# Optimization experiments

Measured on AMD Instinct MI355X. Metric: run time of the kernel, lower is better.

The kernel has to match this reference:

```python
import jax, jax.numpy as jnp
import numpy as np

D = 1024

def setup_inputs() -> dict:
    key = jax.random.key(0)
    ks = jax.random.split(key, 7)
    s = 1.0 / np.sqrt(D)
    x = jax.random.normal(ks[0], (4, 4096, D), dtype=jnp.float32)
    Wi = jax.random.uniform(ks[1], (2 * D, D), jnp.float32, -s, s)   # in_proj weight [2D, D]
    bi = jax.random.uniform(ks[2], (2 * D,), jnp.float32, -s, s)
    Wc = jax.random.uniform(ks[3], (D, 1, 3), jnp.float32, -0.577, 0.577)  # depthwise conv [D,1,3]
    bc = jax.random.uniform(ks[4], (D,), jnp.float32, -0.577, 0.577)
    Wo = jax.random.uniform(ks[5], (D, D), jnp.float32, -s, s)       # out_proj weight [D, D]
    bo = jax.random.uniform(ks[6], (D,), jnp.float32, -s, s)
    return {"x": x, "Wi": Wi, "bi": bi, "Wc": Wc, "bc": bc, "Wo": Wo, "bo": bo}

def _depthwise_conv1d(v, Wc, bc):
    # v: [B, L, D] -> NCH [B, D, L]; kernel [D, 1, 3] (OIH), groups = D; pad 1 both sides
    y = jax.lax.conv_general_dilated(
        v.transpose(0, 2, 1), Wc,
        window_strides=(1,), padding=[(1, 1)],
        dimension_numbers=("NCH", "OIH", "NCH"),
        feature_group_count=v.shape[-1])
    return y.transpose(0, 2, 1) + bc  # [B, L, D]

def reference(x, Wi, bi, Wc, bc, Wo, bo):
    uv = jnp.einsum("bld,ed->ble", x, Wi) + bi        # [B, L, 2D]
    u, v = jnp.split(uv, 2, axis=-1)                   # each [B, L, D]
    y = _depthwise_conv1d(v, Wc, bc)
    y = jax.nn.silu(y) * u                             # fused gate
    return jnp.einsum("bld,ed->ble", y, Wo) + bo       # [B, L, D]
```

## Files before the change

kernel.cpp:

```cpp
#include <hip/hip_runtime.h>
#include <math.h>


typedef __attribute__((ext_vector_type(8))) short short8;
typedef __attribute__((ext_vector_type(4))) float floatx4;

__device__ __forceinline__ float b2f(short s) {
    unsigned int u = ((unsigned int)(unsigned short)s) << 16;
    float f;
    __builtin_memcpy(&f, &u, 4);
    return f;
}

__device__ __forceinline__ short f2b(float f) {
    unsigned int u;
    __builtin_memcpy(&u, &f, 4);
    u += 0x7fffu + ((u >> 16) & 1u);
    return (short)(u >> 16);
}

__device__ __forceinline__ void gl_lds16(const short* g, short* l) {
    __builtin_amdgcn_global_load_lds(
        (const __attribute__((address_space(1))) unsigned int*)g,
        (__attribute__((address_space(3))) unsigned int*)l,
        16, 0, 0);
}

__global__ __launch_bounds__(256) void cvt_all(
    const float* __restrict__ x, const float* __restrict__ Wi,
    const float* __restrict__ Wo, short* __restrict__ xb,
    short* __restrict__ Wib, short* __restrict__ Wob)
{
    constexpr int n1 = 16384 * 1024 / 8;
    constexpr int n2 = 2048 * 1024 / 8;
    constexpr int n3 = 1024 * 1024 / 8;
    int i = blockIdx.x * 256 + threadIdx.x;
    const float* src;
    short* dst;
    int j;
    if (i < n1)           { src = x;  dst = xb;  j = i; }
    else if (i < n1 + n2) { src = Wi; dst = Wib; j = i - n1; }
    else if (i < n1 + n2 + n3) { src = Wo; dst = Wob; j = i - n1 - n2; }
    else return;
    float4 a = ((const float4*)src)[2 * j];
    float4 b = ((const float4*)src)[2 * j + 1];
    short8 o;
    o[0] = f2b(a.x); o[1] = f2b(a.y); o[2] = f2b(a.z); o[3] = f2b(a.w);
    o[4] = f2b(b.x); o[5] = f2b(b.y); o[6] = f2b(b.z); o[7] = f2b(b.w);
    ((short8*)dst)[j] = o;
}

template <bool OUTF32>
__global__ __launch_bounds__(256, 3) void gemm_bt(
    const short* __restrict__ A, const short* __restrict__ B,
    const float* __restrict__ bias, void* __restrict__ Cv,
    int lda, int ldb, int ldc)
{
    constexpr int K = 1024;
    __shared__ __attribute__((aligned(16))) short As[128 * 64];
    __shared__ __attribute__((aligned(16))) short Bs[128 * 64];

    const int tid  = threadIdx.x;
    const int wave = tid >> 6;
    const int lane = tid & 63;
    const int mBase = blockIdx.y * 128;
    const int nBase = blockIdx.x * 128;

    floatx4 acc[4][4];
#pragma unroll
    for (int i = 0; i < 4; i++)
#pragma unroll
        for (int j = 0; j < 4; j++) acc[i][j] = {0.f, 0.f, 0.f, 0.f};

    const int sRow = wave * 32 + (lane >> 3);
    const int sg   = (((lane & 7) ^ ((lane >> 3) & 7))) * 8;
    const short* gA = A + (size_t)(mBase + sRow) * lda + sg;
    const short* gB = B + (size_t)(nBase + sRow) * ldb + sg;
    short* lA = &As[(wave * 32) * 64];
    short* lB = &Bs[(wave * 32) * 64];

    const int mq = (wave & 1) * 64;
    const int nq = (wave >> 1) * 64;
    const int fRow = lane & 15;
    const int lg   = lane >> 4;
    const int p0   = ((lg ^ (fRow & 7))) * 8;

    for (int k0 = 0; k0 < K; k0 += 64) {
        __syncthreads();
#pragma unroll
        for (int j = 0; j < 4; j++) {
            gl_lds16(gA + (size_t)(8 * j) * lda + k0, lA + 8 * j * 64);
            gl_lds16(gB + (size_t)(8 * j) * ldb + k0, lB + 8 * j * 64);
        }
        __syncthreads();

#pragma unroll
        for (int h = 0; h < 2; h++) {
            const int po = p0 ^ (h * 32);
            short8 a[4], b[4];
#pragma unroll
            for (int mi = 0; mi < 4; mi++)
                a[mi] = *(const short8*)&As[(mq + mi * 16 + fRow) * 64 + po];
#pragma unroll
            for (int ni = 0; ni < 4; ni++)
                b[ni] = *(const short8*)&Bs[(nq + ni * 16 + fRow) * 64 + po];
#pragma unroll
            for (int mi = 0; mi < 4; mi++)
#pragma unroll
                for (int ni = 0; ni < 4; ni++)
                    acc[mi][ni] = __builtin_amdgcn_mfma_f32_16x16x32_bf16(
                        a[mi], b[ni], acc[mi][ni], 0, 0, 0);
        }
    }

    const int colq = lane & 15;
    const int rowq = (lane >> 4) * 4;
#pragma unroll
    for (int ni = 0; ni < 4; ni++) {
        const int col = nBase + nq + ni * 16 + colq;
        const float bv = bias[col];
#pragma unroll
        for (int mi = 0; mi < 4; mi++) {
            const int row = mBase + mq + mi * 16 + rowq;
#pragma unroll
            for (int r = 0; r < 4; r++) {
                float v = acc[mi][ni][r] + bv;
                if (OUTF32)
                    ((float*)Cv)[(size_t)(row + r) * ldc + col] = v;
                else
                    ((short*)Cv)[(size_t)(row + r) * ldc + col] = f2b(v);
            }
        }
    }
}

__global__ __launch_bounds__(256) void conv_gate(
    const short* __restrict__ uv, const float* __restrict__ Wc,
    const float* __restrict__ bc, short* __restrict__ yb)
{
    const int idx = blockIdx.x * 256 + threadIdx.x;
    const int d8 = idx & 127;
    const int m  = idx >> 7;
    const int l  = m & 4095;
    const int d  = d8 * 8;

    float w[24];
#pragma unroll
    for (int q = 0; q < 6; q++)
        *(float4*)&w[q * 4] = ((const float4*)(Wc + d * 3))[q];
    float bcv[8];
    *(float4*)&bcv[0] = ((const float4*)(bc + d))[0];
    *(float4*)&bcv[4] = ((const float4*)(bc + d))[1];

    const size_t rowu = (size_t)m * 2048 + d;
    const size_t rowv = rowu + 1024;

    const short8 z = {0, 0, 0, 0, 0, 0, 0, 0};
    const short8 us = *(const short8*)(uv + rowu);
    const short8 vc = *(const short8*)(uv + rowv);
    const short8 vm = (l > 0)    ? *(const short8*)(uv + rowv - 2048) : z;
    const short8 vp = (l < 4095) ? *(const short8*)(uv + rowv + 2048) : z;

    short8 outv;
#pragma unroll
    for (int j = 0; j < 8; j++) {
        float y = b2f(vm[j]) * w[j * 3 + 0]
                + b2f(vc[j]) * w[j * 3 + 1]
                + b2f(vp[j]) * w[j * 3 + 2]
                + bcv[j];
        float sil = y / (1.0f + expf(-y));
        outv[j] = f2b(sil * b2f(us[j]));
    }
    *(short8*)(yb + (size_t)m * 1024 + d) = outv;
}

extern "C" void kernel_launch(void* const* d_in, const int* in_sizes, int n_in,
                              void* d_out, int out_size, void* d_ws, size_t ws_size,
                              hipStream_t stream)
{
    const float* x  = (const float*)d_in[0];
    const float* Wi = (const float*)d_in[1];
    const float* bi = (const float*)d_in[2];
    const float* Wc = (const float*)d_in[3];
    const float* bc = (const float*)d_in[4];
    const float* Wo = (const float*)d_in[5];
    const float* bo = (const float*)d_in[6];
    float* out = (float*)d_out;

    short* wsS = (short*)d_ws;
    short* uv  = wsS;
    short* xb  = uv + (size_t)16384 * 2048;
    short* Wib = xb + (size_t)16384 * 1024;
    short* Wob = Wib + (size_t)2048 * 1024;

    dim3 blk(256);

    constexpr int nCvt = (16384 * 1024 + 2048 * 1024 + 1024 * 1024) / 8;
    cvt_all<<<(nCvt + 255) / 256, blk, 0, stream>>>(x, Wi, Wo, xb, Wib, Wob);

    dim3 g1(2048 / 128, 16384 / 128);
    gemm_bt<false><<<g1, blk, 0, stream>>>(xb, Wib, bi, uv, 1024, 1024, 2048);

    conv_gate<<<(16384 * 128) / 256, blk, 0, stream>>>(uv, Wc, bc, xb);

    dim3 g2(1024 / 128, 16384 / 128);
    gemm_bt<true><<<g2, blk, 0, stream>>>(xb, Wob, bo, out, 1024, 1024, 1024);
}
```

Baseline: 281.9 us.

## Double-buffer GEMM LDS tiles and group block order for L2 reuse

```diff
diff --git a/kernel.cpp b/kernel.cpp
--- a/kernel.cpp
+++ b/kernel.cpp
@@ -51,20 +51,25 @@
 }
 
 template <bool OUTF32>
-__global__ __launch_bounds__(256, 3) void gemm_bt(
+__global__ __launch_bounds__(256, 2) void gemm_bt(
     const short* __restrict__ A, const short* __restrict__ B,
     const float* __restrict__ bias, void* __restrict__ Cv,
-    int lda, int ldb, int ldc)
+    int lda, int ldb, int ldc, int numN)
 {
     constexpr int K = 1024;
-    __shared__ __attribute__((aligned(16))) short As[128 * 64];
-    __shared__ __attribute__((aligned(16))) short Bs[128 * 64];
+    constexpr int NITER = K / 64;
+    __shared__ __attribute__((aligned(16))) short As[2][128 * 64];
+    __shared__ __attribute__((aligned(16))) short Bs[2][128 * 64];
+
+    const int pid   = blockIdx.x;
+    const int group = pid / (8 * numN);
+    const int rem   = pid % (8 * numN);
+    const int mBase = (group * 8 + (rem & 7)) * 128;
+    const int nBase = (rem >> 3) * 128;
 
     const int tid  = threadIdx.x;
     const int wave = tid >> 6;
     const int lane = tid & 63;
-    const int mBase = blockIdx.y * 128;
-    const int nBase = blockIdx.x * 128;
 
     floatx4 acc[4][4];
 #pragma unroll
@@ -76,8 +81,7 @@
     const int sg   = (((lane & 7) ^ ((lane >> 3) & 7))) * 8;
     const short* gA = A + (size_t)(mBase + sRow) * lda + sg;
     const short* gB = B + (size_t)(nBase + sRow) * ldb + sg;
-    short* lA = &As[(wave * 32) * 64];
-    short* lB = &Bs[(wave * 32) * 64];
+    const int ldsOff = (wave * 32) * 64;
 
     const int mq = (wave & 1) * 64;
     const int nq = (wave >> 1) * 64;
@@ -85,14 +89,25 @@
     const int lg   = lane >> 4;
     const int p0   = ((lg ^ (fRow & 7))) * 8;
 
-    for (int k0 = 0; k0 < K; k0 += 64) {
+#pragma unroll
+    for (int j = 0; j < 4; j++) {
+        gl_lds16(gA + (size_t)(8 * j) * lda, &As[0][ldsOff + 8 * j * 64]);
+        gl_lds16(gB + (size_t)(8 * j) * ldb, &Bs[0][ldsOff + 8 * j * 64]);
+    }
+
+#pragma unroll 2
+    for (int it = 0; it < NITER; ++it) {
+        const int buf = it & 1;
+        const int k1 = (it + 1) * 64;
         __syncthreads();
-#pragma unroll
-        for (int j = 0; j < 4; j++) {
-            gl_lds16(gA + (size_t)(8 * j) * lda + k0, lA + 8 * j * 64);
-            gl_lds16(gB + (size_t)(8 * j) * ldb + k0, lB + 8 * j * 64);
+
+        if (k1 < K) {
+#pragma unroll
+            for (int j = 0; j < 4; j++) {
+                gl_lds16(gA + (size_t)(8 * j) * lda + k1, &As[buf ^ 1][ldsOff + 8 * j * 64]);
+                gl_lds16(gB + (size_t)(8 * j) * ldb + k1, &Bs[buf ^ 1][ldsOff + 8 * j * 64]);
+            }
         }
-        __syncthreads();
 
 #pragma unroll
         for (int h = 0; h < 2; h++) {
@@ -100,10 +115,10 @@
             short8 a[4], b[4];
 #pragma unroll
             for (int mi = 0; mi < 4; mi++)
-                a[mi] = *(const short8*)&As[(mq + mi * 16 + fRow) * 64 + po];
+                a[mi] = *(const short8*)&As[buf][(mq + mi * 16 + fRow) * 64 + po];
 #pragma unroll
             for (int ni = 0; ni < 4; ni++)
-                b[ni] = *(const short8*)&Bs[(nq + ni * 16 + fRow) * 64 + po];
+                b[ni] = *(const short8*)&Bs[buf][(nq + ni * 16 + fRow) * 64 + po];
 #pragma unroll
             for (int mi = 0; mi < 4; mi++)
 #pragma unroll
@@ -198,11 +213,9 @@
     constexpr int nCvt = (16384 * 1024 + 2048 * 1024 + 1024 * 1024) / 8;
     cvt_all<<<(nCvt + 255) / 256, blk, 0, stream>>>(x, Wi, Wo, xb, Wib, Wob);
 
-    dim3 g1(2048 / 128, 16384 / 128);
-    gemm_bt<false><<<g1, blk, 0, stream>>>(xb, Wib, bi, uv, 1024, 1024, 2048);
+    gemm_bt<false><<<dim3(128 * 16), blk, 0, stream>>>(xb, Wib, bi, uv, 1024, 1024, 2048, 16);
 
     conv_gate<<<(16384 * 128) / 256, blk, 0, stream>>>(uv, Wc, bc, xb);
 
-    dim3 g2(1024 / 128, 16384 / 128);
-    gemm_bt<true><<<g2, blk, 0, stream>>>(xb, Wob, bo, out, 1024, 1024, 1024);
-}
+    gemm_bt<true><<<dim3(128 * 8), blk, 0, stream>>>(xb, Wob, bo, out, 1024, 1024, 1024, 8);
+}
```

Measured after the change: 285.6 us. No clear change (+1.3%).
